# Performance work log

Measured on AMD Instinct MI355X. Metric: run time of the kernel, lower is better.

The kernel has to match this reference:

```python
import jax, jax.numpy as jnp
import numpy as np

B, N, D = 4, 4096, 1024

def setup_inputs() -> dict:
    key = jax.random.key(0)
    kx, kql, kqr, kk, kv = jax.random.split(key, 5)
    std = 1.0 / D
    return {
        "x": jax.random.normal(kx, (B, N, D), dtype=jnp.float32),
        "w_query_left": jax.random.normal(kql, (D, D), dtype=jnp.float32) * std,
        "w_query_right": jax.random.normal(kqr, (D, D), dtype=jnp.float32) * std,
        "w_key": jax.random.normal(kk, (D, D), dtype=jnp.float32) * std,
        "w_value": jax.random.normal(kv, (D, D), dtype=jnp.float32) * std,
    }

def reference(x, w_query_left, w_query_right, w_key, w_value):
    # Four dxd projections
    query_left = jnp.einsum('bnd,de->bne', x, w_query_left)
    query_right = jnp.einsum('bnd,de->bne', x, w_query_right)
    key = jnp.einsum('bnd,de->bne', x, w_key)
    value = jnp.einsum('bnd,de->bne', x, w_value)
    # Elementwise gate
    query = query_left * query_right
    # Kernelized attention: key^T @ value, then query @ kv  (dropout p=0 in eval)
    kv_attn = jnp.einsum('bnd,bne->bde', key, value)   # [B, D, D]
    linear_attn = jnp.einsum('bnd,bde->bne', query, kv_attn)
    return linear_attn
```

## Files before the change

### kernel.cpp

```cpp
#include <hip/hip_runtime.h>
#include <stdint.h>

typedef short bf16x8 __attribute__((ext_vector_type(8)));
typedef float f32x4 __attribute__((ext_vector_type(4)));

__device__ __forceinline__ float b2f(uint32_t h) {
    return __builtin_bit_cast(float, h << 16);
}
__device__ __forceinline__ uint16_t f2b(float f) {
    uint32_t u = __builtin_bit_cast(uint32_t, f);
    return (uint16_t)((u + 0x7fffu + ((u >> 16) & 1u)) >> 16);
}

__device__ __forceinline__ void gll16(const void* g, void* l) {
    __builtin_amdgcn_global_load_lds(
        (const __attribute__((address_space(1))) uint32_t*)(uintptr_t)g,
        (__attribute__((address_space(3))) uint32_t*)(uint32_t)(uintptr_t)l,
        16, 0, 0);
}

__global__ __launch_bounds__(256) void cvt_f32_bf16(const float4* __restrict__ in,
                                                    uint2* __restrict__ out, int nvec) {
    int i = blockIdx.x * 256 + threadIdx.x;
    if (i >= nvec) return;
    float4 v = in[i];
    uint2 o;
    o.x = (uint32_t)f2b(v.x) | ((uint32_t)f2b(v.y) << 16);
    o.y = (uint32_t)f2b(v.z) | ((uint32_t)f2b(v.w) << 16);
    out[i] = o;
}

struct Ptr4 { const float* p[4]; };

__global__ __launch_bounds__(256) void tr_w(Ptr4 wp, uint16_t* __restrict__ out) {
    const float* in = wp.p[blockIdx.z];
    uint16_t* o = out + (size_t)blockIdx.z * 1048576;
    __shared__ uint16_t tile[64][68];
    int t = threadIdx.x;
    int r0 = blockIdx.y * 64, c0 = blockIdx.x * 64;
    for (int p = 0; p < 4; p++) {
        int row = p * 16 + (t >> 4);
        int c4 = (t & 15) * 4;
        float4 v = *(const float4*)&in[(size_t)(r0 + row) * 1024 + c0 + c4];
        tile[row][c4 + 0] = f2b(v.x);
        tile[row][c4 + 1] = f2b(v.y);
        tile[row][c4 + 2] = f2b(v.z);
        tile[row][c4 + 3] = f2b(v.w);
    }
    __syncthreads();
    for (int p = 0; p < 4; p++) {
        int a = p * 16 + (t >> 4);
        int b4 = (t & 15) * 4;
        uint32_t x0 = tile[b4 + 0][a], x1 = tile[b4 + 1][a];
        uint32_t x2 = tile[b4 + 2][a], x3 = tile[b4 + 3][a];
        uint2 pk;
        pk.x = x0 | (x1 << 16);
        pk.y = x2 | (x3 << 16);
        *(uint2*)&o[(size_t)(c0 + a) * 1024 + r0 + b4] = pk;
    }
}

union SmemU {
    struct { uint16_t lA[128 * 32]; uint16_t lB1[128 * 32]; uint16_t lB2[128 * 32]; } s;
    uint16_t tr[4][64][68];
};

template <int MODE>
__global__ __launch_bounds__(256, 2) void proj2(const uint16_t* __restrict__ A,
                                                const uint16_t* __restrict__ B1,
                                                const uint16_t* __restrict__ B2,
                                                uint16_t* __restrict__ C1,
                                                uint16_t* __restrict__ C2) {
    __shared__ SmemU u;
    const int K = 1024;
    const int t = threadIdx.x;
    const int wave = t >> 6;
    const int lane = t & 63;
    const int m0 = blockIdx.y * 128;
    const int n0 = blockIdx.x * 128;
    const int wm = (wave >> 1) * 64;
    const int wn = (wave & 1) * 64;

    const uint16_t* gA0 = A + (size_t)(m0 + (t >> 2)) * K + (t & 3) * 8;
    const uint16_t* gB1 = B1 + (size_t)(n0 + (t >> 2)) * K + (t & 3) * 8;
    const uint16_t* gB2 = B2 + (size_t)(n0 + (t >> 2)) * K + (t & 3) * 8;
    uint16_t* lA0 = u.s.lA + wave * 512;
    uint16_t* lA1 = u.s.lA + 2048 + wave * 512;
    uint16_t* lB10 = u.s.lB1 + wave * 512;
    uint16_t* lB11 = u.s.lB1 + 2048 + wave * 512;
    uint16_t* lB20 = u.s.lB2 + wave * 512;
    uint16_t* lB21 = u.s.lB2 + 2048 + wave * 512;

    f32x4 acc1[4][4] = {};
    f32x4 acc2[4][4] = {};

    const int arow = wm + (lane & 15);
    const int brow = wn + (lane & 15);
    const int koff = (lane >> 4) * 8;

    for (int k0 = 0; k0 < K; k0 += 32) {
        __syncthreads();
        gll16(gA0 + k0, lA0);
        gll16(gA0 + (size_t)64 * K + k0, lA1);
        gll16(gB1 + k0, lB10);
        gll16(gB1 + (size_t)64 * K + k0, lB11);
        gll16(gB2 + k0, lB20);
        gll16(gB2 + (size_t)64 * K + k0, lB21);
        __syncthreads();

        bf16x8 af[4], b1f[4], b2f_[4];
#pragma unroll
        for (int i = 0; i < 4; i++)
            af[i] = *(const bf16x8*)&u.s.lA[(arow + i * 16) * 32 + koff];
#pragma unroll
        for (int i = 0; i < 4; i++)
            b1f[i] = *(const bf16x8*)&u.s.lB1[(brow + i * 16) * 32 + koff];
#pragma unroll
        for (int i = 0; i < 4; i++)
            b2f_[i] = *(const bf16x8*)&u.s.lB2[(brow + i * 16) * 32 + koff];
#pragma unroll
        for (int i = 0; i < 4; i++)
#pragma unroll
            for (int j = 0; j < 4; j++) {
                acc1[i][j] = __builtin_amdgcn_mfma_f32_16x16x32_bf16(af[i], b1f[i * 0 + j],
                                                                     acc1[i][j], 0, 0, 0);
                acc2[i][j] = __builtin_amdgcn_mfma_f32_16x16x32_bf16(af[i], b2f_[j],
                                                                     acc2[i][j], 0, 0, 0);
            }
    }

    if (MODE == 0) {
        const int crow = m0 + wm + (lane >> 4) * 4;
        const int ccol = n0 + wn + (lane & 15);
#pragma unroll
        for (int i = 0; i < 4; i++)
#pragma unroll
            for (int j = 0; j < 4; j++)
#pragma unroll
                for (int r = 0; r < 4; r++) {
                    float g = acc1[i][j][r] * acc2[i][j][r];
                    C1[(size_t)(crow + i * 16 + r) * 1024 + ccol + j * 16] = f2b(g);
                }
    } else {
        __syncthreads();
        const int bofs = (m0 >> 12) * 4194304;
        const int tok0 = (m0 & 4095) + wm;
        const int fbase = n0 + wn;
        uint16_t* outs[2] = {C1, C2};
        for (int s = 0; s < 2; s++) {
            f32x4(*acc)[4] = (s == 0) ? acc1 : acc2;
#pragma unroll
            for (int i = 0; i < 4; i++)
#pragma unroll
                for (int j = 0; j < 4; j++) {
                    int col = j * 16 + (lane & 15);
                    int row0 = i * 16 + (lane >> 4) * 4;
                    uint32_t lo = (uint32_t)f2b(acc[i][j][0]) | ((uint32_t)f2b(acc[i][j][1]) << 16);
                    uint32_t hi = (uint32_t)f2b(acc[i][j][2]) | ((uint32_t)f2b(acc[i][j][3]) << 16);
                    uint2 pk; pk.x = lo; pk.y = hi;
                    *(uint2*)&u.tr[wave][col][row0] = pk;
                }
            __builtin_amdgcn_s_waitcnt(0);
            uint16_t* O = outs[s] + bofs;
#pragma unroll
            for (int dd = 0; dd < 16; dd++) {
                int f = dd * 4 + (lane >> 4);
                int t4 = (lane & 15) * 4;
                uint2 v = *(const uint2*)&u.tr[wave][f][t4];
                *(uint2*)&O[(size_t)(fbase + f) * 4096 + tok0 + t4] = v;
            }
            __builtin_amdgcn_s_waitcnt(0);
        }
    }
}

template <int OUT_BF16>
__global__ __launch_bounds__(256) void gemm_bt(const uint16_t* __restrict__ A,
                                               const uint16_t* __restrict__ Bt,
                                               void* __restrict__ C,
                                               int K, int ldc,
                                               long long sA, long long sB, long long sC) {
    const uint16_t* Ab = A + (size_t)blockIdx.z * sA;
    const uint16_t* Bb = Bt + (size_t)blockIdx.z * sB;

    __shared__ uint16_t lA[128 * 32];
    __shared__ uint16_t lB[128 * 32];

    const int t = threadIdx.x;
    const int wave = t >> 6;
    const int lane = t & 63;
    const int m0 = blockIdx.y * 128;
    const int n0 = blockIdx.x * 128;
    const int wm = (wave >> 1) * 64;
    const int wn = (wave & 1) * 64;

    const uint16_t* gA0 = Ab + (size_t)(m0 + (t >> 2)) * K + (t & 3) * 8;
    const uint16_t* gB0 = Bb + (size_t)(n0 + (t >> 2)) * K + (t & 3) * 8;
    uint16_t* lA0 = lA + wave * 512;
    uint16_t* lA1 = lA + 2048 + wave * 512;
    uint16_t* lB0 = lB + wave * 512;
    uint16_t* lB1 = lB + 2048 + wave * 512;

    f32x4 acc[4][4] = {};

    const int arow = wm + (lane & 15);
    const int brow = wn + (lane & 15);
    const int koff = (lane >> 4) * 8;

    for (int k0 = 0; k0 < K; k0 += 32) {
        __syncthreads();
        gll16(gA0 + k0, lA0);
        gll16(gA0 + (size_t)64 * K + k0, lA1);
        gll16(gB0 + k0, lB0);
        gll16(gB0 + (size_t)64 * K + k0, lB1);
        __syncthreads();

        bf16x8 af[4], bfr[4];
#pragma unroll
        for (int i = 0; i < 4; i++)
            af[i] = *(const bf16x8*)&lA[(arow + i * 16) * 32 + koff];
#pragma unroll
        for (int i = 0; i < 4; i++)
            bfr[i] = *(const bf16x8*)&lB[(brow + i * 16) * 32 + koff];
#pragma unroll
        for (int i = 0; i < 4; i++)
#pragma unroll
            for (int j = 0; j < 4; j++)
                acc[i][j] = __builtin_amdgcn_mfma_f32_16x16x32_bf16(af[i], bfr[j],
                                                                    acc[i][j], 0, 0, 0);
    }

    const int crow = m0 + wm + (lane >> 4) * 4;
    const int ccol = n0 + wn + (lane & 15);
    if (OUT_BF16) {
        uint16_t* Cb = (uint16_t*)C + (size_t)blockIdx.z * sC;
#pragma unroll
        for (int i = 0; i < 4; i++)
#pragma unroll
            for (int j = 0; j < 4; j++)
#pragma unroll
                for (int r = 0; r < 4; r++)
                    Cb[(size_t)(crow + i * 16 + r) * ldc + ccol + j * 16] = f2b(acc[i][j][r]);
    } else {
        float* Cb = (float*)C + (size_t)blockIdx.z * sC;
#pragma unroll
        for (int i = 0; i < 4; i++)
#pragma unroll
            for (int j = 0; j < 4; j++)
#pragma unroll
                for (int r = 0; r < 4; r++)
                    Cb[(size_t)(crow + i * 16 + r) * ldc + ccol + j * 16] = acc[i][j][r];
    }
}

__global__ __launch_bounds__(256) void gemm_kv_splitk(const uint16_t* __restrict__ VT,
                                                      const uint16_t* __restrict__ KT,
                                                      float* __restrict__ P) {
    const int z = blockIdx.z;
    const int batch = z >> 2, ks = z & 3;
    const uint16_t* Ab = VT + (size_t)batch * 4194304 + ks * 1024;
    const uint16_t* Bb = KT + (size_t)batch * 4194304 + ks * 1024;

    __shared__ uint16_t lA[128 * 32];
    __shared__ uint16_t lB[128 * 32];

    const int t = threadIdx.x;
    const int wave = t >> 6;
    const int lane = t & 63;
    const int m0 = blockIdx.y * 128;
    const int n0 = blockIdx.x * 128;
    const int wm = (wave >> 1) * 64;
    const int wn = (wave & 1) * 64;

    const uint16_t* gA0 = Ab + (size_t)(m0 + (t >> 2)) * 4096 + (t & 3) * 8;
    const uint16_t* gB0 = Bb + (size_t)(n0 + (t >> 2)) * 4096 + (t & 3) * 8;
    uint16_t* lA0 = lA + wave * 512;
    uint16_t* lA1 = lA + 2048 + wave * 512;
    uint16_t* lB0 = lB + wave * 512;
    uint16_t* lB1 = lB + 2048 + wave * 512;

    f32x4 acc[4][4] = {};

    const int arow = wm + (lane & 15);
    const int brow = wn + (lane & 15);
    const int koff = (lane >> 4) * 8;

    for (int k0 = 0; k0 < 1024; k0 += 32) {
        __syncthreads();
        gll16(gA0 + k0, lA0);
        gll16(gA0 + (size_t)64 * 4096 + k0, lA1);
        gll16(gB0 + k0, lB0);
        gll16(gB0 + (size_t)64 * 4096 + k0, lB1);
        __syncthreads();

        bf16x8 af[4], bfr[4];
#pragma unroll
        for (int i = 0; i < 4; i++)
            af[i] = *(const bf16x8*)&lA[(arow + i * 16) * 32 + koff];
#pragma unroll
        for (int i = 0; i < 4; i++)
            bfr[i] = *(const bf16x8*)&lB[(brow + i * 16) * 32 + koff];
#pragma unroll
        for (int i = 0; i < 4; i++)
#pragma unroll
            for (int j = 0; j < 4; j++)
                acc[i][j] = __builtin_amdgcn_mfma_f32_16x16x32_bf16(af[i], bfr[j],
                                                                    acc[i][j], 0, 0, 0);
    }

    float* Pb = P + (size_t)z * 1048576;
    const int crow = m0 + wm + (lane >> 4) * 4;
    const int ccol = n0 + wn + (lane & 15);
#pragma unroll
    for (int i = 0; i < 4; i++)
#pragma unroll
        for (int j = 0; j < 4; j++)
#pragma unroll
            for (int r = 0; r < 4; r++)
                Pb[(size_t)(crow + i * 16 + r) * 1024 + ccol + j * 16] = acc[i][j][r];
}

__global__ __launch_bounds__(256) void reduce_kv(const float4* __restrict__ P,
                                                 uint2* __restrict__ kvT) {
    int i = blockIdx.x * 256 + threadIdx.x;
    int b = i >> 18;
    int r = i & 262143;
    const float4* base = P + (size_t)b * 1048576 + r;
    float4 s0 = base[0];
    float4 s1 = base[262144];
    float4 s2 = base[524288];
    float4 s3 = base[786432];
    float x = s0.x + s1.x + s2.x + s3.x;
    float y = s0.y + s1.y + s2.y + s3.y;
    float zz = s0.z + s1.z + s2.z + s3.z;
    float w = s0.w + s1.w + s2.w + s3.w;
    uint2 o;
    o.x = (uint32_t)f2b(x) | ((uint32_t)f2b(y) << 16);
    o.y = (uint32_t)f2b(zz) | ((uint32_t)f2b(w) << 16);
    kvT[i] = o;
}

extern "C" void kernel_launch(void* const* d_in, const int* in_sizes, int n_in,
                              void* d_out, int out_size, void* d_ws, size_t ws_size,
                              hipStream_t stream) {
    const float* x = (const float*)d_in[0];

    uint16_t* ws = (uint16_t*)d_ws;
    uint16_t* xb  = ws;
    float*    kvP = (float*)d_ws;
    uint16_t* Wt  = ws + 33554432;
    uint16_t* kvT = Wt;
    uint16_t* Q   = ws + 37748736;
    uint16_t* KT  = ws + 54525952;
    uint16_t* VT  = ws + 71303168;

    cvt_f32_bf16<<<16384, 256, 0, stream>>>((const float4*)x, (uint2*)xb, 4194304);

    Ptr4 wp;
    wp.p[0] = (const float*)d_in[1];
    wp.p[1] = (const float*)d_in[2];
    wp.p[2] = (const float*)d_in[3];
    wp.p[3] = (const float*)d_in[4];
    tr_w<<<dim3(16, 16, 4), 256, 0, stream>>>(wp, Wt);

    proj2<0><<<dim3(8, 128), 256, 0, stream>>>(xb, Wt, Wt + 1048576, Q, nullptr);

    proj2<1><<<dim3(8, 128), 256, 0, stream>>>(xb, Wt + 2097152, Wt + 3145728, KT, VT);

    gemm_kv_splitk<<<dim3(8, 8, 16), 256, 0, stream>>>(VT, KT, kvP);

    reduce_kv<<<4096, 256, 0, stream>>>((const float4*)kvP, (uint2*)kvT);

    gemm_bt<0><<<dim3(8, 32, 4), 256, 0, stream>>>(Q, kvT, d_out, 1024, 1024,
                                                   4194304LL, 1048576LL, 4194304LL);
}
```

Measured before the change: 407.4 us.

## Pack four projection weights into one interleaved matrix and add LDS swizzle

The weight transposes are now interleaved so that one projection kernel computes all four projections as a single 16384x4096 GEMM. Each 128-wide N tile pairs left/right query halves (or key/value halves) across waves, and the query gating product is exchanged through LDS. This replaces two dual-B launches with one larger single-B launch. An XOR swizzle is also applied to the LDS tile layout in all GEMMs to cut bank conflicts on fragment reads. In exchange, the gate epilogue needs an extra LDS round trip and barrier, and each block covers only 64 output columns per projection.

```diff
diff --git a/kernel.cpp b/kernel.cpp
--- a/kernel.cpp
+++ b/kernel.cpp
@@ -4,9 +4,6 @@
 typedef short bf16x8 __attribute__((ext_vector_type(8)));
 typedef float f32x4 __attribute__((ext_vector_type(4)));
 
-__device__ __forceinline__ float b2f(uint32_t h) {
-    return __builtin_bit_cast(float, h << 16);
-}
 __device__ __forceinline__ uint16_t f2b(float f) {
     uint32_t u = __builtin_bit_cast(uint32_t, f);
     return (uint16_t)((u + 0x7fffu + ((u >> 16) & 1u)) >> 16);
@@ -32,12 +29,13 @@
 
 struct Ptr4 { const float* p[4]; };
 
-__global__ __launch_bounds__(256) void tr_w(Ptr4 wp, uint16_t* __restrict__ out) {
-    const float* in = wp.p[blockIdx.z];
-    uint16_t* o = out + (size_t)blockIdx.z * 1048576;
+__global__ __launch_bounds__(256) void tr_w_packed(Ptr4 wp, uint16_t* __restrict__ out) {
+    const int m = blockIdx.z;
+    const float* in = wp.p[m];
     __shared__ uint16_t tile[64][68];
     int t = threadIdx.x;
-    int r0 = blockIdx.y * 64, c0 = blockIdx.x * 64;
+    int r0 = blockIdx.y * 64;
+    int c0 = blockIdx.x * 64;
     for (int p = 0; p < 4; p++) {
         int row = p * 16 + (t >> 4);
         int c4 = (t & 15) * 4;
@@ -48,6 +46,7 @@
         tile[row][c4 + 3] = f2b(v.w);
     }
     __syncthreads();
+    const int prow_base = (m >> 1) * 2048 + blockIdx.x * 128 + (m & 1) * 64;
     for (int p = 0; p < 4; p++) {
         int a = p * 16 + (t >> 4);
         int b4 = (t & 15) * 4;
@@ -56,23 +55,22 @@
         uint2 pk;
         pk.x = x0 | (x1 << 16);
         pk.y = x2 | (x3 << 16);
-        *(uint2*)&o[(size_t)(c0 + a) * 1024 + r0 + b4] = pk;
-    }
-}
-
-union SmemU {
-    struct { uint16_t lA[128 * 32]; uint16_t lB1[128 * 32]; uint16_t lB2[128 * 32]; } s;
+        *(uint2*)&out[(size_t)(prow_base + a) * 1024 + r0 + b4] = pk;
+    }
+}
+
+union SmemP {
+    struct { uint16_t lA[4096]; uint16_t lB[4096]; } s;
+    float ep[2][4096];
     uint16_t tr[4][64][68];
 };
 
-template <int MODE>
-__global__ __launch_bounds__(256, 2) void proj2(const uint16_t* __restrict__ A,
-                                                const uint16_t* __restrict__ B1,
-                                                const uint16_t* __restrict__ B2,
-                                                uint16_t* __restrict__ C1,
-                                                uint16_t* __restrict__ C2) {
-    __shared__ SmemU u;
-    const int K = 1024;
+__global__ __launch_bounds__(256) void proj_packed(const uint16_t* __restrict__ A,
+                                                   const uint16_t* __restrict__ B,
+                                                   uint16_t* __restrict__ Q,
+                                                   uint16_t* __restrict__ KT,
+                                                   uint16_t* __restrict__ VT) {
+    __shared__ SmemP u;
     const int t = threadIdx.x;
     const int wave = t >> 6;
     const int lane = t & 63;
@@ -81,110 +79,110 @@
     const int wm = (wave >> 1) * 64;
     const int wn = (wave & 1) * 64;
 
-    const uint16_t* gA0 = A + (size_t)(m0 + (t >> 2)) * K + (t & 3) * 8;
-    const uint16_t* gB1 = B1 + (size_t)(n0 + (t >> 2)) * K + (t & 3) * 8;
-    const uint16_t* gB2 = B2 + (size_t)(n0 + (t >> 2)) * K + (t & 3) * 8;
+    const int gcol = (((t & 3) ^ ((t >> 3) & 3)) * 8);
+    const uint16_t* gA0 = A + (size_t)(m0 + (t >> 2)) * 1024 + gcol;
+    const uint16_t* gB0 = B + (size_t)(n0 + (t >> 2)) * 1024 + gcol;
     uint16_t* lA0 = u.s.lA + wave * 512;
     uint16_t* lA1 = u.s.lA + 2048 + wave * 512;
-    uint16_t* lB10 = u.s.lB1 + wave * 512;
-    uint16_t* lB11 = u.s.lB1 + 2048 + wave * 512;
-    uint16_t* lB20 = u.s.lB2 + wave * 512;
-    uint16_t* lB21 = u.s.lB2 + 2048 + wave * 512;
-
-    f32x4 acc1[4][4] = {};
-    f32x4 acc2[4][4] = {};
+    uint16_t* lB0 = u.s.lB + wave * 512;
+    uint16_t* lB1 = u.s.lB + 2048 + wave * 512;
+
+    f32x4 acc[4][4] = {};
 
     const int arow = wm + (lane & 15);
     const int brow = wn + (lane & 15);
-    const int koff = (lane >> 4) * 8;
-
-    for (int k0 = 0; k0 < K; k0 += 32) {
+    const int swz = (((lane >> 4) ^ (((lane & 15) >> 1) & 3)) * 8);
+
+    for (int k0 = 0; k0 < 1024; k0 += 32) {
         __syncthreads();
         gll16(gA0 + k0, lA0);
-        gll16(gA0 + (size_t)64 * K + k0, lA1);
-        gll16(gB1 + k0, lB10);
-        gll16(gB1 + (size_t)64 * K + k0, lB11);
-        gll16(gB2 + k0, lB20);
-        gll16(gB2 + (size_t)64 * K + k0, lB21);
-        __syncthreads();
-
-        bf16x8 af[4], b1f[4], b2f_[4];
-#pragma unroll
-        for (int i = 0; i < 4; i++)
-            af[i] = *(const bf16x8*)&u.s.lA[(arow + i * 16) * 32 + koff];
-#pragma unroll
-        for (int i = 0; i < 4; i++)
-            b1f[i] = *(const bf16x8*)&u.s.lB1[(brow + i * 16) * 32 + koff];
-#pragma unroll
-        for (int i = 0; i < 4; i++)
-            b2f_[i] = *(const bf16x8*)&u.s.lB2[(brow + i * 16) * 32 + koff];
+        gll16(gA0 + (size_t)64 * 1024 + k0, lA1);
+        gll16(gB0 + k0, lB0);
+        gll16(gB0 + (size_t)64 * 1024 + k0, lB1);
+        __syncthreads();
+
+        bf16x8 af[4], bfr[4];
+#pragma unroll
+        for (int i = 0; i < 4; i++)
+            af[i] = *(const bf16x8*)&u.s.lA[(arow + i * 16) * 32 + swz];
+#pragma unroll
+        for (int i = 0; i < 4; i++)
+            bfr[i] = *(const bf16x8*)&u.s.lB[(brow + i * 16) * 32 + swz];
+#pragma unroll
+        for (int i = 0; i < 4; i++)
+#pragma unroll
+            for (int j = 0; j < 4; j++)
+                acc[i][j] = __builtin_amdgcn_mfma_f32_16x16x32_bf16(af[i], bfr[j],
+                                                                    acc[i][j], 0, 0, 0);
+    }
+
+    __syncthreads();
+
+    const int rl = (lane >> 4) * 4;
+    const int cl = lane & 15;
+
+    if (blockIdx.x < 16) {
+        if (wave & 1) {
+            float* ep = u.ep[wave >> 1];
+#pragma unroll
+            for (int i = 0; i < 4; i++)
+#pragma unroll
+                for (int j = 0; j < 4; j++)
+#pragma unroll
+                    for (int r = 0; r < 4; r++)
+                        ep[(i * 16 + rl + r) * 64 + j * 16 + cl] = acc[i][j][r];
+        }
+        __syncthreads();
+        if (!(wave & 1)) {
+            const float* ep = u.ep[wave >> 1];
+            const int e0 = blockIdx.x * 64;
+#pragma unroll
+            for (int i = 0; i < 4; i++)
+#pragma unroll
+                for (int j = 0; j < 4; j++)
+#pragma unroll
+                    for (int r = 0; r < 4; r++) {
+                        float g = acc[i][j][r] * ep[(i * 16 + rl + r) * 64 + j * 16 + cl];
+                        Q[(size_t)(m0 + wm + i * 16 + rl + r) * 1024 + e0 + j * 16 + cl] = f2b(g);
+                    }
+        }
+    } else {
+        const int batch = m0 >> 12;
+        const int tok0 = (m0 & 4095) + wm;
+        const int e0 = (blockIdx.x - 16) * 64;
+        uint16_t* O = ((wave & 1) ? VT : KT) + (size_t)batch * 4194304;
 #pragma unroll
         for (int i = 0; i < 4; i++)
 #pragma unroll
             for (int j = 0; j < 4; j++) {
-                acc1[i][j] = __builtin_amdgcn_mfma_f32_16x16x32_bf16(af[i], b1f[i * 0 + j],
-                                                                     acc1[i][j], 0, 0, 0);
-                acc2[i][j] = __builtin_amdgcn_mfma_f32_16x16x32_bf16(af[i], b2f_[j],
-                                                                     acc2[i][j], 0, 0, 0);
+                int col = j * 16 + cl;
+                int row0 = i * 16 + rl;
+                uint2 pk;
+                pk.x = (uint32_t)f2b(acc[i][j][0]) | ((uint32_t)f2b(acc[i][j][1]) << 16);
+                pk.y = (uint32_t)f2b(acc[i][j][2]) | ((uint32_t)f2b(acc[i][j][3]) << 16);
+                *(uint2*)&u.tr[wave][col][row0] = pk;
             }
-    }
-
-    if (MODE == 0) {
-        const int crow = m0 + wm + (lane >> 4) * 4;
-        const int ccol = n0 + wn + (lane & 15);
-#pragma unroll
-        for (int i = 0; i < 4; i++)
-#pragma unroll
-            for (int j = 0; j < 4; j++)
-#pragma unroll
-                for (int r = 0; r < 4; r++) {
-                    float g = acc1[i][j][r] * acc2[i][j][r];
-                    C1[(size_t)(crow + i * 16 + r) * 1024 + ccol + j * 16] = f2b(g);
-                }
-    } else {
-        __syncthreads();
-        const int bofs = (m0 >> 12) * 4194304;
-        const int tok0 = (m0 & 4095) + wm;
-        const int fbase = n0 + wn;
-        uint16_t* outs[2] = {C1, C2};
-        for (int s = 0; s < 2; s++) {
-            f32x4(*acc)[4] = (s == 0) ? acc1 : acc2;
-#pragma unroll
-            for (int i = 0; i < 4; i++)
-#pragma unroll
-                for (int j = 0; j < 4; j++) {
-                    int col = j * 16 + (lane & 15);
-                    int row0 = i * 16 + (lane >> 4) * 4;
-                    uint32_t lo = (uint32_t)f2b(acc[i][j][0]) | ((uint32_t)f2b(acc[i][j][1]) << 16);
-                    uint32_t hi = (uint32_t)f2b(acc[i][j][2]) | ((uint32_t)f2b(acc[i][j][3]) << 16);
-                    uint2 pk; pk.x = lo; pk.y = hi;
-                    *(uint2*)&u.tr[wave][col][row0] = pk;
-                }
-            __builtin_amdgcn_s_waitcnt(0);
-            uint16_t* O = outs[s] + bofs;
-#pragma unroll
-            for (int dd = 0; dd < 16; dd++) {
-                int f = dd * 4 + (lane >> 4);
-                int t4 = (lane & 15) * 4;
-                uint2 v = *(const uint2*)&u.tr[wave][f][t4];
-                *(uint2*)&O[(size_t)(fbase + f) * 4096 + tok0 + t4] = v;
-            }
-            __builtin_amdgcn_s_waitcnt(0);
+        __builtin_amdgcn_s_waitcnt(0);
+#pragma unroll
+        for (int dd = 0; dd < 16; dd++) {
+            int f = dd * 4 + (lane >> 4);
+            int t4 = cl * 4;
+            uint2 v = *(const uint2*)&u.tr[wave][f][t4];
+            *(uint2*)&O[(size_t)(e0 + f) * 4096 + tok0 + t4] = v;
         }
     }
 }
 
-template <int OUT_BF16>
-__global__ __launch_bounds__(256) void gemm_bt(const uint16_t* __restrict__ A,
-                                               const uint16_t* __restrict__ Bt,
-                                               void* __restrict__ C,
-                                               int K, int ldc,
-                                               long long sA, long long sB, long long sC) {
-    const uint16_t* Ab = A + (size_t)blockIdx.z * sA;
-    const uint16_t* Bb = Bt + (size_t)blockIdx.z * sB;
-
-    __shared__ uint16_t lA[128 * 32];
-    __shared__ uint16_t lB[128 * 32];
+__global__ __launch_bounds__(256) void gemm_kv_splitk(const uint16_t* __restrict__ VT,
+                                                      const uint16_t* __restrict__ KT,
+                                                      float* __restrict__ P) {
+    const int z = blockIdx.z;
+    const int batch = z >> 2, ks = z & 3;
+    const uint16_t* Ab = VT + (size_t)batch * 4194304 + ks * 1024;
+    const uint16_t* Bb = KT + (size_t)batch * 4194304 + ks * 1024;
+
+    __shared__ uint16_t lA[4096];
+    __shared__ uint16_t lB[4096];
 
     const int t = threadIdx.x;
     const int wave = t >> 6;
@@ -194,8 +192,9 @@
     const int wm = (wave >> 1) * 64;
     const int wn = (wave & 1) * 64;
 
-    const uint16_t* gA0 = Ab + (size_t)(m0 + (t >> 2)) * K + (t & 3) * 8;
-    const uint16_t* gB0 = Bb + (size_t)(n0 + (t >> 2)) * K + (t & 3) * 8;
+    const int gcol = (((t & 3) ^ ((t >> 3) & 3)) * 8);
+    const uint16_t* gA0 = Ab + (size_t)(m0 + (t >> 2)) * 4096 + gcol;
+    const uint16_t* gB0 = Bb + (size_t)(n0 + (t >> 2)) * 4096 + gcol;
     uint16_t* lA0 = lA + wave * 512;
     uint16_t* lA1 = lA + 2048 + wave * 512;
     uint16_t* lB0 = lB + wave * 512;
@@ -205,85 +204,7 @@
 
     const int arow = wm + (lane & 15);
     const int brow = wn + (lane & 15);
-    const int koff = (lane >> 4) * 8;
-
-    for (int k0 = 0; k0 < K; k0 += 32) {
-        __syncthreads();
-        gll16(gA0 + k0, lA0);
-        gll16(gA0 + (size_t)64 * K + k0, lA1);
-        gll16(gB0 + k0, lB0);
-        gll16(gB0 + (size_t)64 * K + k0, lB1);
-        __syncthreads();
-
-        bf16x8 af[4], bfr[4];
-#pragma unroll
-        for (int i = 0; i < 4; i++)
-            af[i] = *(const bf16x8*)&lA[(arow + i * 16) * 32 + koff];
-#pragma unroll
-        for (int i = 0; i < 4; i++)
-            bfr[i] = *(const bf16x8*)&lB[(brow + i * 16) * 32 + koff];
-#pragma unroll
-        for (int i = 0; i < 4; i++)
-#pragma unroll
-            for (int j = 0; j < 4; j++)
-                acc[i][j] = __builtin_amdgcn_mfma_f32_16x16x32_bf16(af[i], bfr[j],
-                                                                    acc[i][j], 0, 0, 0);
-    }
-
-    const int crow = m0 + wm + (lane >> 4) * 4;
-    const int ccol = n0 + wn + (lane & 15);
-    if (OUT_BF16) {
-        uint16_t* Cb = (uint16_t*)C + (size_t)blockIdx.z * sC;
-#pragma unroll
-        for (int i = 0; i < 4; i++)
-#pragma unroll
-            for (int j = 0; j < 4; j++)
-#pragma unroll
-                for (int r = 0; r < 4; r++)
-                    Cb[(size_t)(crow + i * 16 + r) * ldc + ccol + j * 16] = f2b(acc[i][j][r]);
-    } else {
-        float* Cb = (float*)C + (size_t)blockIdx.z * sC;
-#pragma unroll
-        for (int i = 0; i < 4; i++)
-#pragma unroll
-            for (int j = 0; j < 4; j++)
-#pragma unroll
-                for (int r = 0; r < 4; r++)
-                    Cb[(size_t)(crow + i * 16 + r) * ldc + ccol + j * 16] = acc[i][j][r];
-    }
-}
-
-__global__ __launch_bounds__(256) void gemm_kv_splitk(const uint16_t* __restrict__ VT,
-                                                      const uint16_t* __restrict__ KT,
-                                                      float* __restrict__ P) {
-    const int z = blockIdx.z;
-    const int batch = z >> 2, ks = z & 3;
-    const uint16_t* Ab = VT + (size_t)batch * 4194304 + ks * 1024;
-    const uint16_t* Bb = KT + (size_t)batch * 4194304 + ks * 1024;
-
-    __shared__ uint16_t lA[128 * 32];
-    __shared__ uint16_t lB[128 * 32];
-
-    const int t = threadIdx.x;
-    const int wave = t >> 6;
-    const int lane = t & 63;
-    const int m0 = blockIdx.y * 128;
-    const int n0 = blockIdx.x * 128;
-    const int wm = (wave >> 1) * 64;
-    const int wn = (wave & 1) * 64;
-
-    const uint16_t* gA0 = Ab + (size_t)(m0 + (t >> 2)) * 4096 + (t & 3) * 8;
-    const uint16_t* gB0 = Bb + (size_t)(n0 + (t >> 2)) * 4096 + (t & 3) * 8;
-    uint16_t* lA0 = lA + wave * 512;
-    uint16_t* lA1 = lA + 2048 + wave * 512;
-    uint16_t* lB0 = lB + wave * 512;
-    uint16_t* lB1 = lB + 2048 + wave * 512;
-
-    f32x4 acc[4][4] = {};
-
-    const int arow = wm + (lane & 15);
-    const int brow = wn + (lane & 15);
-    const int koff = (lane >> 4) * 8;
+    const int swz = (((lane >> 4) ^ (((lane & 15) >> 1) & 3)) * 8);
 
     for (int k0 = 0; k0 < 1024; k0 += 32) {
         __syncthreads();
@@ -296,10 +217,10 @@
         bf16x8 af[4], bfr[4];
 #pragma unroll
         for (int i = 0; i < 4; i++)
-            af[i] = *(const bf16x8*)&lA[(arow + i * 16) * 32 + koff];
-#pragma unroll
-        for (int i = 0; i < 4; i++)
-            bfr[i] = *(const bf16x8*)&lB[(brow + i * 16) * 32 + koff];
+            af[i] = *(const bf16x8*)&lA[(arow + i * 16) * 32 + swz];
+#pragma unroll
+        for (int i = 0; i < 4; i++)
+            bfr[i] = *(const bf16x8*)&lB[(brow + i * 16) * 32 + swz];
 #pragma unroll
         for (int i = 0; i < 4; i++)
 #pragma unroll
@@ -340,6 +261,72 @@
     kvT[i] = o;
 }
 
+__global__ __launch_bounds__(256) void gemm_out(const uint16_t* __restrict__ A,
+                                                const uint16_t* __restrict__ Bt,
+                                                float* __restrict__ C) {
+    const uint16_t* Ab = A + (size_t)blockIdx.z * 4194304;
+    const uint16_t* Bb = Bt + (size_t)blockIdx.z * 1048576;
+
+    __shared__ uint16_t lA[4096];
+    __shared__ uint16_t lB[4096];
+
+    const int t = threadIdx.x;
+    const int wave = t >> 6;
+    const int lane = t & 63;
+    const int m0 = blockIdx.y * 128;
+    const int n0 = blockIdx.x * 128;
+    const int wm = (wave >> 1) * 64;
+    const int wn = (wave & 1) * 64;
+
+    const int gcol = (((t & 3) ^ ((t >> 3) & 3)) * 8);
+    const uint16_t* gA0 = Ab + (size_t)(m0 + (t >> 2)) * 1024 + gcol;
+    const uint16_t* gB0 = Bb + (size_t)(n0 + (t >> 2)) * 1024 + gcol;
+    uint16_t* lA0 = lA + wave * 512;
+    uint16_t* lA1 = lA + 2048 + wave * 512;
+    uint16_t* lB0 = lB + wave * 512;
+    uint16_t* lB1 = lB + 2048 + wave * 512;
+
+    f32x4 acc[4][4] = {};
+
+    const int arow = wm + (lane & 15);
+    const int brow = wn + (lane & 15);
+    const int swz = (((lane >> 4) ^ (((lane & 15) >> 1) & 3)) * 8);
+
+    for (int k0 = 0; k0 < 1024; k0 += 32) {
+        __syncthreads();
+        gll16(gA0 + k0, lA0);
+        gll16(gA0 + (size_t)64 * 1024 + k0, lA1);
+        gll16(gB0 + k0, lB0);
+        gll16(gB0 + (size_t)64 * 1024 + k0, lB1);
+        __syncthreads();
+
+        bf16x8 af[4], bfr[4];
+#pragma unroll
+        for (int i = 0; i < 4; i++)
+            af[i] = *(const bf16x8*)&lA[(arow + i * 16) * 32 + swz];
+#pragma unroll
+        for (int i = 0; i < 4; i++)
+            bfr[i] = *(const bf16x8*)&lB[(brow + i * 16) * 32 + swz];
+#pragma unroll
+        for (int i = 0; i < 4; i++)
+#pragma unroll
+            for (int j = 0; j < 4; j++)
+                acc[i][j] = __builtin_amdgcn_mfma_f32_16x16x32_bf16(af[i], bfr[j],
+                                                                    acc[i][j], 0, 0, 0);
+    }
+
+    float* Cb = C + (size_t)blockIdx.z * 4194304;
+    const int crow = m0 + wm + (lane >> 4) * 4;
+    const int ccol = n0 + wn + (lane & 15);
+#pragma unroll
+    for (int i = 0; i < 4; i++)
+#pragma unroll
+        for (int j = 0; j < 4; j++)
+#pragma unroll
+            for (int r = 0; r < 4; r++)
+                Cb[(size_t)(crow + i * 16 + r) * 1024 + ccol + j * 16] = acc[i][j][r];
+}
+
 extern "C" void kernel_launch(void* const* d_in, const int* in_sizes, int n_in,
                               void* d_out, int out_size, void* d_ws, size_t ws_size,
                               hipStream_t stream) {
@@ -361,16 +348,13 @@
     wp.p[1] = (const float*)d_in[2];
     wp.p[2] = (const float*)d_in[3];
     wp.p[3] = (const float*)d_in[4];
-    tr_w<<<dim3(16, 16, 4), 256, 0, stream>>>(wp, Wt);
-
-    proj2<0><<<dim3(8, 128), 256, 0, stream>>>(xb, Wt, Wt + 1048576, Q, nullptr);
-
-    proj2<1><<<dim3(8, 128), 256, 0, stream>>>(xb, Wt + 2097152, Wt + 3145728, KT, VT);
+    tr_w_packed<<<dim3(16, 16, 4), 256, 0, stream>>>(wp, Wt);
+
+    proj_packed<<<dim3(32, 128), 256, 0, stream>>>(xb, Wt, Q, KT, VT);
 
     gemm_kv_splitk<<<dim3(8, 8, 16), 256, 0, stream>>>(VT, KT, kvP);
 
     reduce_kv<<<4096, 256, 0, stream>>>((const float4*)kvP, (uint2*)kvT);
 
-    gemm_bt<0><<<dim3(8, 32, 4), 256, 0, stream>>>(Q, kvT, d_out, 1024, 1024,
-                                                   4194304LL, 1048576LL, 4194304LL);
-}
+    gemm_out<<<dim3(8, 32, 4), 256, 0, stream>>>(Q, kvT, (float*)d_out);
+}
```

After: 551.7 us. +35.4%, slower.
